# Kernel tuning notes

Measured on AMD Instinct MI355X. Metric: run time of the kernel, lower is better.

## Reference

```python
import jax, jax.numpy as jnp
import numpy as np

DIM = 1024
HEADS = 16
HEAD_DIM = DIM // HEADS
HIDDEN = int(DIM * 4.0)
EPS = 1e-5


def layernorm(x, w, b):
    m = jnp.mean(x, axis=-1, keepdims=True)
    v = jnp.var(x, axis=-1, keepdims=True)
    return (x - m) * jax.lax.rsqrt(v + EPS) * w + b


def apply_rope(t, pos):
    # t: [B, H, S, D], pos: [B, S] int
    half = t.shape[-1] // 2
    inv_freq = 1.0 / (10000.0 ** (jnp.arange(half, dtype=jnp.float32) / half))
    ang = pos.astype(jnp.float32)[:, None, :, None] * inv_freq  # [B,1,S,half]
    cos = jnp.cos(ang)
    sin = jnp.sin(ang)
    t1, t2 = t[..., :half], t[..., half:]
    return jnp.concatenate([t1 * cos - t2 * sin, t2 * cos + t1 * sin], axis=-1)


def setup_inputs() -> dict:
    key = jax.random.key(0)
    ks = jax.random.split(key, 10)
    B, S = 2, 2048
    x = jax.random.normal(ks[0], (B, S, DIM), dtype=jnp.float32)
    pos = jnp.sort(jax.random.randint(ks[1], (B, S), 0, 2048), axis=-1).astype(jnp.int32)
    def lin(k, fi, fo):
        return jax.random.normal(k, (fi, fo), dtype=jnp.float32) / np.sqrt(fi)
    return {
        "x": x,
        "pos": pos,
        "ln1_w": jnp.ones((DIM,), jnp.float32),
        "ln1_b": jnp.zeros((DIM,), jnp.float32),
        "qkv_w": lin(ks[2], DIM, 3 * DIM),
        "qkv_b": jnp.zeros((3 * DIM,), jnp.float32),
        "o_w": lin(ks[3], DIM, DIM),
        "o_b": jnp.zeros((DIM,), jnp.float32),
        "ln2_w": jnp.ones((DIM,), jnp.float32),
        "ln2_b": jnp.zeros((DIM,), jnp.float32),
        "mlp_w1": lin(ks[4], DIM, HIDDEN),
        "mlp_b1": jnp.zeros((HIDDEN,), jnp.float32),
        "mlp_w2": lin(ks[5], HIDDEN, DIM),
        "mlp_b2": jnp.zeros((DIM,), jnp.float32),
    }


def reference(x, pos, ln1_w, ln1_b, qkv_w, qkv_b, o_w, o_b, ln2_w, ln2_b, mlp_w1, mlp_b1, mlp_w2, mlp_b2):
    B, S, C = x.shape
    scale = HEAD_DIM ** -0.5
    xn = layernorm(x, ln1_w, ln1_b)
    qkv = (xn @ qkv_w + qkv_b).reshape(B, S, 3, HEADS, HEAD_DIM)
    qkv = jnp.transpose(qkv, (2, 0, 3, 1, 4))  # [3,B,H,S,D]
    q, k, v = qkv[0], qkv[1], qkv[2]
    q = apply_rope(q, pos)
    k = apply_rope(k, pos)
    scores = jnp.einsum("bhsd,bhtd->bhst", q, k) * scale
    probs = jax.nn.softmax(scores, axis=-1)
    attn = jnp.einsum("bhst,bhtd->bhsd", probs, v)
    attn = jnp.transpose(attn, (0, 2, 1, 3)).reshape(B, S, C)
    x = x + attn @ o_w + o_b
    xn2 = layernorm(x, ln2_w, ln2_b)
    h = jax.nn.gelu(xn2 @ mlp_w1 + mlp_b1, approximate=False)
    x = x + h @ mlp_w2 + mlp_b2
    return x
```

## Files before the change

### kernel.cpp

```cpp
#include <hip/hip_runtime.h>
#include <hip/hip_bf16.h>
#include <math.h>

#define DIMC 1024
#define HEADS 16
#define HD 64
#define HIDDEN 4096
#define BATCH 2
#define SEQ 2048
#define TOK (BATCH*SEQ)

typedef unsigned short u16;
typedef __attribute__((ext_vector_type(8))) short short8;
typedef __attribute__((ext_vector_type(4))) float f32x4;

__device__ __forceinline__ u16 f2bf(float f) {
  unsigned u = __float_as_uint(f);
  u += 0x7fff + ((u >> 16) & 1);
  return (u16)(u >> 16);
}
__device__ __forceinline__ float bf2f(u16 h) {
  return __uint_as_float(((unsigned)h) << 16);
}

__device__ __forceinline__ void gl_lds16(const void* g, void* l) {
  __builtin_amdgcn_global_load_lds(
      (__attribute__((address_space(1))) void*)g,
      (__attribute__((address_space(3))) void*)l, 16, 0, 0);
}

__device__ __forceinline__ const short8* lds_row128(const u16* base, int row, int chunk) {
  return (const short8*)((const char*)base + row * 128 + (((chunk) ^ (row & 7)) << 4));
}

__global__ __launch_bounds__(256) void ln_kernel(
    const float* __restrict__ x, const float* __restrict__ w,
    const float* __restrict__ b, u16* __restrict__ out)
{
  int row = blockIdx.x, tid = threadIdx.x;
  const float4* xr = (const float4*)(x + (size_t)row * DIMC);
  float4 v = xr[tid];
  float s = v.x + v.y + v.z + v.w;
  float s2 = v.x*v.x + v.y*v.y + v.z*v.z + v.w*v.w;
  for (int off = 32; off > 0; off >>= 1) {
    s  += __shfl_down(s, off);
    s2 += __shfl_down(s2, off);
  }
  __shared__ float red[8];
  int lane = tid & 63, wv = tid >> 6;
  if (lane == 0) { red[wv] = s; red[4 + wv] = s2; }
  __syncthreads();
  float S  = red[0] + red[1] + red[2] + red[3];
  float S2 = red[4] + red[5] + red[6] + red[7];
  float mean = S * (1.f / DIMC);
  float var  = S2 * (1.f / DIMC) - mean * mean;
  float inv  = rsqrtf(var + 1e-5f);
  int base = tid * 4;
  float vv[4] = {v.x, v.y, v.z, v.w};
#pragma unroll
  for (int j = 0; j < 4; ++j)
    out[(size_t)row * DIMC + base + j] = f2bf((vv[j] - mean) * inv * w[base + j] + b[base + j]);
}

__global__ __launch_bounds__(256) void transpose_cast(
    const float* __restrict__ W, u16* __restrict__ Wt, int K, int N)
{
  __shared__ float t[32][33];
  int n0 = blockIdx.x * 32, k0 = blockIdx.y * 32;
  for (int r = threadIdx.y; r < 32; r += 8)
    t[r][threadIdx.x] = W[(size_t)(k0 + r) * N + n0 + threadIdx.x];
  __syncthreads();
  for (int r = threadIdx.y; r < 32; r += 8)
    Wt[(size_t)(n0 + r) * K + k0 + threadIdx.x] = f2bf(t[threadIdx.x][r]);
}

template<int EPI, int BM>
__global__ __launch_bounds__(256) void gemm_bt(
    const u16* __restrict__ A, const u16* __restrict__ Bt,
    const float* __restrict__ bias, const float* __restrict__ res,
    u16* __restrict__ outb, float* __restrict__ outf,
    int M, int N, int K)
{
  constexpr int AMM  = BM / 32;
  constexpr int HALF = BM / 2;
  constexpr int AJ   = BM / 32;
  constexpr int ASZ  = BM * 64;
  constexpr int BSZ  = 128 * 64;
  __shared__ u16 shm[(BM + 128) * 64 * 2];
  int tid = threadIdx.x;
  int lane = tid & 63, w = tid >> 6;
  int wr = w >> 1, wc = w & 1;

  int nwg = gridDim.x * gridDim.y;
  int orig = blockIdx.y * gridDim.x + blockIdx.x;
  int wg = (orig & 7) * (nwg >> 3) + (orig >> 3);
  int gi = wg >> 4, wi = wg & 15;
  int gx4 = gridDim.x >> 2;
  int bx = (gi % gx4) * 4 + (wi & 3);
  int by = (gi / gx4) * 4 + (wi >> 2);
  int m0 = by * BM, n0 = bx * 128;

  f32x4 acc[AMM][4] = {};

  int offA[AJ], offB[4];
#pragma unroll
  for (int j = 0; j < AJ; ++j) {
    int p = tid + j * 256, row = p >> 3, cl = (p & 7) ^ (row & 7);
    offA[j] = (m0 + row) * K + cl * 8;
  }
#pragma unroll
  for (int j = 0; j < 4; ++j) {
    int p = tid + j * 256, row = p >> 3, cl = (p & 7) ^ (row & 7);
    offB[j] = (n0 + row) * K + cl * 8;
  }
  int rofs = lane & 15, q4 = lane >> 4;
  int NT = K >> 6;

  auto stage = [&](int buf, int t) {
    u16* Ab = shm + buf * ASZ;
    u16* Bb = shm + 2 * ASZ + buf * BSZ;
#pragma unroll
    for (int j = 0; j < AJ; ++j)
      gl_lds16(A + offA[j] + t * 64, Ab + (tid + j * 256) * 8);
#pragma unroll
    for (int j = 0; j < 4; ++j)
      gl_lds16(Bt + offB[j] + t * 64, Bb + (tid + j * 256) * 8);
  };
  auto compute = [&](int buf) {
    const char* Ab = (const char*)(shm + buf * ASZ);
    const char* Bb = (const char*)(shm + 2 * ASZ + buf * BSZ);
    short8 af[AMM][2], bfr[4][2];
#pragma unroll
    for (int mm = 0; mm < AMM; ++mm)
#pragma unroll
      for (int kk = 0; kk < 2; ++kk) {
        int row = wr * HALF + mm * 16 + rofs;
        af[mm][kk] = *(const short8*)(Ab + row * 128 +
                                      ((((kk << 2) | q4) ^ (row & 7)) << 4));
      }
#pragma unroll
    for (int nn = 0; nn < 4; ++nn)
#pragma unroll
      for (int kk = 0; kk < 2; ++kk) {
        int row = wc * 64 + nn * 16 + rofs;
        bfr[nn][kk] = *(const short8*)(Bb + row * 128 +
                                       ((((kk << 2) | q4) ^ (row & 7)) << 4));
      }
#pragma unroll
    for (int kk = 0; kk < 2; ++kk)
#pragma unroll
      for (int mm = 0; mm < AMM; ++mm)
#pragma unroll
        for (int nn = 0; nn < 4; ++nn)
          acc[mm][nn] = __builtin_amdgcn_mfma_f32_16x16x32_bf16(
              af[mm][kk], bfr[nn][kk], acc[mm][nn], 0, 0, 0);
  };

  stage(0, 0);
  __syncthreads();
  int cur = 0;
  for (int t = 0; t < NT; ++t) {
    if (t + 1 < NT) stage(cur ^ 1, t + 1);
    compute(cur);
    __syncthreads();
    cur ^= 1;
  }

  if (EPI == 0 || EPI == 1) {
    u16* C = shm;
#pragma unroll
    for (int nn = 0; nn < 4; ++nn) {
      int ccol = wc * 64 + nn * 16 + rofs;
      float bv = bias[n0 + ccol];
#pragma unroll
      for (int mm = 0; mm < AMM; ++mm)
#pragma unroll
        for (int r = 0; r < 4; ++r) {
          int crow = wr * HALF + mm * 16 + q4 * 4 + r;
          float v = acc[mm][nn][r] + bv;
          if (EPI == 1) v = 0.5f * v * (1.f + erff(v * 0.70710678118f));
          C[crow * 128 + ccol] = f2bf(v);
        }
    }
    __syncthreads();
    for (int c = tid; c < BM * 16; c += 256) {
      int row = c >> 4, off = (c & 15) * 8;
      *(short8*)(outb + (size_t)(m0 + row) * N + n0 + off) = *(const short8*)&C[row * 128 + off];
    }
  } else {
    float* Cf = (float*)shm;
#pragma unroll
    for (int p = 0; p < 2; ++p) {
      if (wr == p) {
#pragma unroll
        for (int nn = 0; nn < 4; ++nn) {
          int ccol = wc * 64 + nn * 16 + rofs;
          float bv = bias[n0 + ccol];
#pragma unroll
          for (int mm = 0; mm < AMM; ++mm)
#pragma unroll
            for (int r = 0; r < 4; ++r)
              Cf[(mm * 16 + q4 * 4 + r) * 128 + ccol] = acc[mm][nn][r] + bv;
        }
      }
      __syncthreads();
      for (int c = tid; c < HALF * 32; c += 256) {
        int row = c >> 5, off = (c & 31) * 4;
        size_t idx = (size_t)(m0 + p * HALF + row) * N + n0 + off;
        float4 rv = *(const float4*)(res + idx);
        float4 cv = *(const float4*)&Cf[row * 128 + off];
        cv.x += rv.x; cv.y += rv.y; cv.z += rv.z; cv.w += rv.w;
        *(float4*)(outf + idx) = cv;
      }
      __syncthreads();
    }
  }
}

__global__ __launch_bounds__(256) void rope_split(
    const u16* __restrict__ qkv, const int* __restrict__ pos,
    u16* __restrict__ Q, u16* __restrict__ Kk, u16* __restrict__ Vt)
{
  int st = blockIdx.x, bh = blockIdx.y;
  int b = bh >> 4, hh = bh & 15;
  int s0 = st * 64;
  int tid = threadIdx.x;
  __shared__ u16 vtile[64][72];

  for (int i = tid; i < 64 * 32; i += 256) {
    int sl = i >> 5, dp = i & 31;
    int s = s0 + sl;
    float p = (float)pos[b * SEQ + s];
    float freq = exp2f((float)dp * -0.4152410118609203f);
    float ang = p * freq;
    float sn, c;
    __sincosf(ang, &sn, &c);
    const u16* qr = qkv + (size_t)(b * SEQ + s) * 3072 + hh * 64;
    float q1 = bf2f(qr[dp]),        q2 = bf2f(qr[dp + 32]);
    float k1 = bf2f(qr[1024 + dp]), k2 = bf2f(qr[1024 + dp + 32]);
    size_t ob = ((size_t)bh * SEQ + s) * HD;
    const float QS = 0.18033688011112042f;
    Q[ob + dp]       = f2bf((q1 * c - q2 * sn) * QS);
    Q[ob + dp + 32]  = f2bf((q2 * c + q1 * sn) * QS);
    Kk[ob + dp]      = f2bf(k1 * c - k2 * sn);
    Kk[ob + dp + 32] = f2bf(k2 * c + k1 * sn);
  }
  for (int i = tid; i < 64 * 64; i += 256) {
    int sl = i >> 6, d = i & 63;
    vtile[d][sl] = qkv[(size_t)(b * SEQ + s0 + sl) * 3072 + 2048 + hh * 64 + d];
  }
  __syncthreads();
  for (int i = tid; i < 64 * 64; i += 256) {
    int d = i >> 6, sl = i & 63;
    Vt[((size_t)bh * HD + d) * SEQ + s0 + sl] = vtile[d][sl];
  }
}

__global__ __launch_bounds__(256) void attn_kernel(
    const u16* __restrict__ Q, const u16* __restrict__ K,
    const u16* __restrict__ Vt, u16* __restrict__ O)
{
  __shared__ u16 Ks[2][64 * 64];
  __shared__ u16 Vs[2][64 * 64];
  __shared__ u16 Ps[4 * 16 * 64];
  int qt = blockIdx.x, bh = blockIdx.y;
  int b = bh >> 4, hh = bh & 15;
  const u16* Qp = Q + ((size_t)bh * SEQ + qt * 64) * HD;
  const u16* Kp = K + (size_t)bh * SEQ * HD;
  const u16* Vp = Vt + (size_t)bh * HD * SEQ;
  int tid = threadIdx.x, lane = tid & 63, w = tid >> 6;
  int rofs = lane & 15, q4 = lane >> 4;
  int kofs = q4 * 8;

  short8 aq0 = *(const short8*)&Qp[(w * 16 + rofs) * HD + kofs];
  short8 aq1 = *(const short8*)&Qp[(w * 16 + rofs) * HD + 32 + kofs];

  short8 ones;
#pragma unroll
  for (int j = 0; j < 8; ++j) ones[j] = (short)0x3F80;

  f32x4 o[4] = {};
  f32x4 lsum = {};

  int srow = tid >> 3;
  int sg0 = ((tid & 7) ^ (srow & 7)) * 8;
  u16* pw = &Ps[w * 16 * 64];

#define A_STAGE(BUF, T0) do { \
    gl_lds16(Kp + (size_t)((T0) + srow) * HD + sg0, &Ks[BUF][tid * 8]); \
    gl_lds16(Kp + (size_t)((T0) + 32 + srow) * HD + sg0, &Ks[BUF][tid * 8 + 2048]); \
    gl_lds16(Vp + (size_t)srow * SEQ + (T0) + sg0, &Vs[BUF][tid * 8]); \
    gl_lds16(Vp + (size_t)(32 + srow) * SEQ + (T0) + sg0, &Vs[BUF][tid * 8 + 2048]); \
  } while (0)

  auto tile = [&](const u16* KsB, const u16* VsB) {
    f32x4 s[4] = {};
#pragma unroll
    for (int n = 0; n < 4; ++n) {
      int krow = n * 16 + rofs;
      short8 bk0 = *lds_row128(KsB, krow, q4);
      short8 bk1 = *lds_row128(KsB, krow, 4 + q4);
      s[n] = __builtin_amdgcn_mfma_f32_16x16x32_bf16(aq0, bk0, s[n], 0, 0, 0);
      s[n] = __builtin_amdgcn_mfma_f32_16x16x32_bf16(aq1, bk1, s[n], 0, 0, 0);
    }
#pragma unroll
    for (int n = 0; n < 4; ++n)
#pragma unroll
      for (int r = 0; r < 4; ++r) {
        int prow = q4 * 4 + r;
        int pbyte = (n * 16 + rofs) * 2;
        float p = __builtin_amdgcn_exp2f(s[n][r]);
        *(u16*)((char*)pw + prow * 128 + (pbyte ^ ((prow & 7) << 4))) = f2bf(p);
      }
    short8 pa0 = *lds_row128(pw, rofs, q4);
    short8 pa1 = *lds_row128(pw, rofs, 4 + q4);
    lsum = __builtin_amdgcn_mfma_f32_16x16x32_bf16(pa0, ones, lsum, 0, 0, 0);
    lsum = __builtin_amdgcn_mfma_f32_16x16x32_bf16(pa1, ones, lsum, 0, 0, 0);
#pragma unroll
    for (int n = 0; n < 4; ++n) {
      int vrow = n * 16 + rofs;
      short8 bv0 = *lds_row128(VsB, vrow, q4);
      short8 bv1 = *lds_row128(VsB, vrow, 4 + q4);
      o[n] = __builtin_amdgcn_mfma_f32_16x16x32_bf16(pa0, bv0, o[n], 0, 0, 0);
      o[n] = __builtin_amdgcn_mfma_f32_16x16x32_bf16(pa1, bv1, o[n], 0, 0, 0);
    }
  };

  A_STAGE(0, 0);
  __syncthreads();
  for (int t0 = 0; t0 < SEQ; t0 += 128) {
    if (t0 + 64 < SEQ) A_STAGE(1, t0 + 64);
    tile(Ks[0], Vs[0]);
    __syncthreads();
    if (t0 + 128 < SEQ) A_STAGE(0, t0 + 128);
    tile(Ks[1], Vs[1]);
    __syncthreads();
  }
#undef A_STAGE

#pragma unroll
  for (int r = 0; r < 4; ++r) {
    float inv = 1.f / lsum[r];
    int lrow = w * 16 + q4 * 4 + r;
#pragma unroll
    for (int n = 0; n < 4; ++n)
      Ps[lrow * 64 + n * 16 + rofs] = f2bf(o[n][r] * inv);
  }
  __syncthreads();
  for (int c = tid; c < 512; c += 256) {
    int row = c >> 3, off = (c & 7) * 8;
    int sq = qt * 64 + row;
    *(short8*)(O + ((size_t)b * SEQ + sq) * DIMC + hh * 64 + off) = *(const short8*)&Ps[row * 64 + off];
  }
}

extern "C" void kernel_launch(void* const* d_in, const int* in_sizes, int n_in,
                              void* d_out, int out_size, void* d_ws, size_t ws_size,
                              hipStream_t stream) {
  const float* x     = (const float*)d_in[0];
  const int*   pos   = (const int*)  d_in[1];
  const float* ln1_w = (const float*)d_in[2];
  const float* ln1_b = (const float*)d_in[3];
  const float* qkv_w = (const float*)d_in[4];
  const float* qkv_b = (const float*)d_in[5];
  const float* o_w   = (const float*)d_in[6];
  const float* o_b   = (const float*)d_in[7];
  const float* ln2_w = (const float*)d_in[8];
  const float* ln2_b = (const float*)d_in[9];
  const float* w1    = (const float*)d_in[10];
  const float* b1    = (const float*)d_in[11];
  const float* w2    = (const float*)d_in[12];
  const float* b2    = (const float*)d_in[13];
  float* out = (float*)d_out;

  char* ws = (char*)d_ws;
  u16* WqkvT = (u16*)(ws + 0);
  u16* WoT   = (u16*)(ws + 6291456);
  u16* W1T   = (u16*)(ws + 8388608);
  u16* W2T   = (u16*)(ws + 16777216);
  u16* xn    = (u16*)(ws + 25165824);
  u16* qkvbf = (u16*)(ws + 33554432);
  u16* Qb    = (u16*)(ws + 58720256);
  u16* Kb    = (u16*)(ws + 67108864);
  u16* Vtb   = (u16*)(ws + 75497472);
  u16* attnb = (u16*)(ws + 83886080);
  u16* hbuf  = (u16*)(ws + 25165824);
  float* x2  = (float*)(ws + 58720256);
  u16* xn2   = (u16*)(ws + 75497472);

  transpose_cast<<<dim3(3072/32, 1024/32), dim3(32, 8), 0, stream>>>(qkv_w, WqkvT, 1024, 3072);
  transpose_cast<<<dim3(1024/32, 1024/32), dim3(32, 8), 0, stream>>>(o_w,  WoT,  1024, 1024);
  transpose_cast<<<dim3(4096/32, 1024/32), dim3(32, 8), 0, stream>>>(w1,   W1T,  1024, 4096);
  transpose_cast<<<dim3(1024/32, 4096/32), dim3(32, 8), 0, stream>>>(w2,   W2T,  4096, 1024);

  ln_kernel<<<TOK, 256, 0, stream>>>(x, ln1_w, ln1_b, xn);
  gemm_bt<0,128><<<dim3(24, 32), 256, 0, stream>>>(xn, WqkvT, qkv_b, nullptr, qkvbf, nullptr, 4096, 3072, 1024);
  rope_split<<<dim3(32, 32), 256, 0, stream>>>(qkvbf, pos, Qb, Kb, Vtb);
  attn_kernel<<<dim3(32, 32), 256, 0, stream>>>(Qb, Kb, Vtb, attnb);
  gemm_bt<2,64><<<dim3(8, 64), 256, 0, stream>>>(attnb, WoT, o_b, x, nullptr, x2, 4096, 1024, 1024);
  ln_kernel<<<TOK, 256, 0, stream>>>(x2, ln2_w, ln2_b, xn2);
  gemm_bt<1,128><<<dim3(32, 32), 256, 0, stream>>>(xn2, W1T, b1, nullptr, hbuf, nullptr, 4096, 4096, 1024);
  gemm_bt<2,64><<<dim3(8, 64), 256, 0, stream>>>(hbuf, W2T, b2, x2, nullptr, out, 4096, 1024, 4096);
}
```

Measured before the change: 256.6 us.

## Add 256x256-tile 8-wave GEMM with XCD-aware remap for QKV and MLP-up

Adds a new gemm8p kernel using 512 threads, 256x256 output tiles, XOR-swizzled LDS filled by direct global-to-LDS loads, and a phased pipeline that interleaves half-K staging with MFMA compute under explicit waitcnt and barrier control. Workgroup IDs are remapped across the 8 XCDs and grouped into 4x4 supertiles to improve L2 reuse. The QKV and first MLP GEMMs now use it, and the old gemm_bt keeps only the residual epilogue. The larger tile raises arithmetic intensity, but with one block per CU the grids of 192 and 256 blocks may fill the machine unevenly, and the hand-tuned waitcnt counts are fragile.

```diff
diff --git a/kernel.cpp b/kernel.cpp
--- a/kernel.cpp
+++ b/kernel.cpp
@@ -72,6 +72,118 @@
   __syncthreads();
   for (int r = threadIdx.y; r < 32; r += 8)
     Wt[(size_t)(n0 + r) * K + k0 + threadIdx.x] = f2bf(t[threadIdx.x][r]);
+}
+
+template<int EPI>
+__global__ __launch_bounds__(512, 1) void gemm8p(
+    const u16* __restrict__ A, const u16* __restrict__ Bt,
+    const float* __restrict__ bias, u16* __restrict__ outb,
+    int M, int N, int K)
+{
+  __shared__ u16 lds[2][2][2][256 * 32];
+  int tid = threadIdx.x;
+  int lane = tid & 63, wid = tid >> 6;
+  int wr = wid >> 2, wn = wid & 3;
+  int rofs = lane & 15, q4 = lane >> 4;
+
+  int nwg = gridDim.x * gridDim.y;
+  int orig = blockIdx.y * gridDim.x + blockIdx.x;
+  int wg = (orig & 7) * (nwg >> 3) + (orig >> 3);
+  int gi = wg >> 4, wi = wg & 15;
+  int gx4 = gridDim.x >> 2;
+  int bx = (gi % gx4) * 4 + (wi & 3);
+  int by = (gi / gx4) * 4 + (wi >> 2);
+  int m0 = by * 256, n0 = bx * 256;
+  int mb = wr * 128, nb = wn * 64;
+
+  f32x4 acc[8][4] = {};
+
+  int p0 = tid, p1 = tid + 512;
+  int r0 = p0 >> 2, c0 = ((p0 & 3) ^ (r0 & 3)) * 8;
+  int r1 = p1 >> 2, c1 = ((p1 & 3) ^ (r1 & 3)) * 8;
+  size_t aoff0 = (size_t)(m0 + r0) * K + c0, aoff1 = (size_t)(m0 + r1) * K + c1;
+  size_t boff0 = (size_t)(n0 + r0) * K + c0, boff1 = (size_t)(n0 + r1) * K + c1;
+
+#define STAGE_A(D_, H_, KC_) do { \
+    gl_lds16(A + aoff0 + (KC_), &lds[D_][0][H_][tid * 8]); \
+    gl_lds16(A + aoff1 + (KC_), &lds[D_][0][H_][(tid + 512) * 8]); } while (0)
+#define STAGE_B(D_, H_, KC_) do { \
+    gl_lds16(Bt + boff0 + (KC_), &lds[D_][1][H_][tid * 8]); \
+    gl_lds16(Bt + boff1 + (KC_), &lds[D_][1][H_][(tid + 512) * 8]); } while (0)
+
+#define PH_COMP(D_, H_, MG_) do { \
+    const char* Ab = (const char*)&lds[D_][0][H_][0]; \
+    const char* Bb = (const char*)&lds[D_][1][H_][0]; \
+    short8 a_[4], b_[4]; \
+    _Pragma("unroll") for (int mm = 0; mm < 4; ++mm) { \
+      int row = mb + ((MG_) * 4 + mm) * 16 + rofs; \
+      a_[mm] = *(const short8*)(Ab + row * 64 + ((q4 ^ (row & 3)) << 4)); \
+    } \
+    _Pragma("unroll") for (int nn = 0; nn < 4; ++nn) { \
+      int row = nb + nn * 16 + rofs; \
+      b_[nn] = *(const short8*)(Bb + row * 64 + ((q4 ^ (row & 3)) << 4)); \
+    } \
+    __builtin_amdgcn_s_setprio(1); \
+    _Pragma("unroll") for (int mm = 0; mm < 4; ++mm) \
+      _Pragma("unroll") for (int nn = 0; nn < 4; ++nn) \
+        acc[(MG_) * 4 + mm][nn] = __builtin_amdgcn_mfma_f32_16x16x32_bf16( \
+            a_[mm], b_[nn], acc[(MG_) * 4 + mm][nn], 0, 0, 0); \
+    __builtin_amdgcn_s_setprio(0); } while (0)
+
+#define VMW(N_) asm volatile("s_waitcnt vmcnt(" #N_ ")" ::: "memory")
+#define SBAR()  do { __builtin_amdgcn_s_barrier(); asm volatile("" ::: "memory"); } while (0)
+
+  int NT = K >> 6;
+  STAGE_A(0, 0, 0); STAGE_B(0, 0, 0); STAGE_A(0, 1, 32); STAGE_B(0, 1, 32);
+
+  for (int t = 0; t < NT; ++t) {
+    int d = t & 1, nx = d ^ 1;
+    int kc = (t + 1) * 64;
+    bool st = (t + 1 < NT);
+    if (st) { STAGE_A(nx, 0, kc); VMW(6); } else { VMW(4); }
+    SBAR();
+    PH_COMP(d, 0, 0);
+    SBAR();
+    if (st) STAGE_B(nx, 0, kc);
+    SBAR();
+    PH_COMP(d, 0, 1);
+    SBAR();
+    if (st) { STAGE_A(nx, 1, kc + 32); VMW(6); } else { VMW(0); }
+    SBAR();
+    PH_COMP(d, 1, 0);
+    SBAR();
+    if (st) STAGE_B(nx, 1, kc + 32);
+    SBAR();
+    PH_COMP(d, 1, 1);
+    SBAR();
+  }
+#undef STAGE_A
+#undef STAGE_B
+#undef PH_COMP
+#undef VMW
+#undef SBAR
+
+  __syncthreads();
+  u16* Ct = &lds[0][0][0][0];
+#pragma unroll
+  for (int nn = 0; nn < 4; ++nn) {
+    int ccol = nb + nn * 16 + rofs;
+    float bv = bias[n0 + ccol];
+#pragma unroll
+    for (int m = 0; m < 8; ++m)
+#pragma unroll
+      for (int r = 0; r < 4; ++r) {
+        int row = mb + m * 16 + q4 * 4 + r;
+        float v = acc[m][nn][r] + bv;
+        if (EPI == 1) v = 0.5f * v * (1.f + erff(v * 0.70710678118f));
+        Ct[row * 256 + ccol] = f2bf(v);
+      }
+  }
+  __syncthreads();
+  for (int c = tid; c < 256 * 32; c += 512) {
+    int row = c >> 5, offb = (c & 31) * 8;
+    *(short8*)(outb + (size_t)(m0 + row) * N + n0 + offb) = *(const short8*)&Ct[row * 256 + offb];
+  }
 }
 
 template<int EPI, int BM>
@@ -166,54 +278,31 @@
     cur ^= 1;
   }
 
-  if (EPI == 0 || EPI == 1) {
-    u16* C = shm;
-#pragma unroll
-    for (int nn = 0; nn < 4; ++nn) {
-      int ccol = wc * 64 + nn * 16 + rofs;
-      float bv = bias[n0 + ccol];
-#pragma unroll
-      for (int mm = 0; mm < AMM; ++mm)
-#pragma unroll
-        for (int r = 0; r < 4; ++r) {
-          int crow = wr * HALF + mm * 16 + q4 * 4 + r;
-          float v = acc[mm][nn][r] + bv;
-          if (EPI == 1) v = 0.5f * v * (1.f + erff(v * 0.70710678118f));
-          C[crow * 128 + ccol] = f2bf(v);
-        }
+  float* Cf = (float*)shm;
+#pragma unroll
+  for (int p = 0; p < 2; ++p) {
+    if (wr == p) {
+#pragma unroll
+      for (int nn = 0; nn < 4; ++nn) {
+        int ccol = wc * 64 + nn * 16 + rofs;
+        float bv = bias[n0 + ccol];
+#pragma unroll
+        for (int mm = 0; mm < AMM; ++mm)
+#pragma unroll
+          for (int r = 0; r < 4; ++r)
+            Cf[(mm * 16 + q4 * 4 + r) * 128 + ccol] = acc[mm][nn][r] + bv;
+      }
     }
     __syncthreads();
-    for (int c = tid; c < BM * 16; c += 256) {
-      int row = c >> 4, off = (c & 15) * 8;
-      *(short8*)(outb + (size_t)(m0 + row) * N + n0 + off) = *(const short8*)&C[row * 128 + off];
+    for (int c = tid; c < HALF * 32; c += 256) {
+      int row = c >> 5, off = (c & 31) * 4;
+      size_t idx = (size_t)(m0 + p * HALF + row) * N + n0 + off;
+      float4 rv = *(const float4*)(res + idx);
+      float4 cv = *(const float4*)&Cf[row * 128 + off];
+      cv.x += rv.x; cv.y += rv.y; cv.z += rv.z; cv.w += rv.w;
+      *(float4*)(outf + idx) = cv;
     }
-  } else {
-    float* Cf = (float*)shm;
-#pragma unroll
-    for (int p = 0; p < 2; ++p) {
-      if (wr == p) {
-#pragma unroll
-        for (int nn = 0; nn < 4; ++nn) {
-          int ccol = wc * 64 + nn * 16 + rofs;
-          float bv = bias[n0 + ccol];
-#pragma unroll
-          for (int mm = 0; mm < AMM; ++mm)
-#pragma unroll
-            for (int r = 0; r < 4; ++r)
-              Cf[(mm * 16 + q4 * 4 + r) * 128 + ccol] = acc[mm][nn][r] + bv;
-        }
-      }
-      __syncthreads();
-      for (int c = tid; c < HALF * 32; c += 256) {
-        int row = c >> 5, off = (c & 31) * 4;
-        size_t idx = (size_t)(m0 + p * HALF + row) * N + n0 + off;
-        float4 rv = *(const float4*)(res + idx);
-        float4 cv = *(const float4*)&Cf[row * 128 + off];
-        cv.x += rv.x; cv.y += rv.y; cv.z += rv.z; cv.w += rv.w;
-        *(float4*)(outf + idx) = cv;
-      }
-      __syncthreads();
-    }
+    __syncthreads();
   }
 }
 
@@ -394,11 +483,11 @@
   transpose_cast<<<dim3(1024/32, 4096/32), dim3(32, 8), 0, stream>>>(w2,   W2T,  4096, 1024);
 
   ln_kernel<<<TOK, 256, 0, stream>>>(x, ln1_w, ln1_b, xn);
-  gemm_bt<0,128><<<dim3(24, 32), 256, 0, stream>>>(xn, WqkvT, qkv_b, nullptr, qkvbf, nullptr, 4096, 3072, 1024);
+  gemm8p<0><<<dim3(12, 16), 512, 0, stream>>>(xn, WqkvT, qkv_b, qkvbf, 4096, 3072, 1024);
   rope_split<<<dim3(32, 32), 256, 0, stream>>>(qkvbf, pos, Qb, Kb, Vtb);
   attn_kernel<<<dim3(32, 32), 256, 0, stream>>>(Qb, Kb, Vtb, attnb);
   gemm_bt<2,64><<<dim3(8, 64), 256, 0, stream>>>(attnb, WoT, o_b, x, nullptr, x2, 4096, 1024, 1024);
   ln_kernel<<<TOK, 256, 0, stream>>>(x2, ln2_w, ln2_b, xn2);
-  gemm_bt<1,128><<<dim3(32, 32), 256, 0, stream>>>(xn2, W1T, b1, nullptr, hbuf, nullptr, 4096, 4096, 1024);
+  gemm8p<1><<<dim3(16, 16), 512, 0, stream>>>(xn2, W1T, b1, hbuf, 4096, 4096, 1024);
   gemm_bt<2,64><<<dim3(8, 64), 256, 0, stream>>>(hbuf, W2T, b2, x2, nullptr, out, 4096, 1024, 4096);
 }
```

Result: slower. 279.1 us (+8.8%).

## Double query tile per attention block and split GEMMs into specialized kernels

Applied to the files above, without the earlier changes.

The attention kernel now handles 128 query rows per block instead of 64, so each K/V tile loaded into LDS is reused by twice as many query rows, and it halves the grid. The 128-row GEMMs (QKV, MLP1) are rewritten as a single-buffered loop with one LDS buffer, in place of the double-buffered stage/compute pipeline. The residual GEMMs are moved into separately named kernels. In exchange, attention carries more accumulator registers per wave and fewer blocks, and the QKV/MLP1 GEMMs lose their overlap of global loads with compute but use less LDS, which may allow higher occupancy.

```diff
diff --git a/kernel.cpp b/kernel.cpp
--- a/kernel.cpp
+++ b/kernel.cpp
@@ -74,19 +74,118 @@
     Wt[(size_t)(n0 + r) * K + k0 + threadIdx.x] = f2bf(t[threadIdx.x][r]);
 }
 
-template<int EPI, int BM>
-__global__ __launch_bounds__(256) void gemm_bt(
+template<int GELU>
+__device__ __forceinline__ void gemm_lin_body(
+    u16* shm, const u16* __restrict__ A, const u16* __restrict__ Bt,
+    const float* __restrict__ bias, u16* __restrict__ outb, int M, int N, int K)
+{
+  int tid = threadIdx.x;
+  int lane = tid & 63, w = tid >> 6;
+  int wr = w >> 1, wc = w & 1;
+
+  int nwg = gridDim.x * gridDim.y;
+  int orig = blockIdx.y * gridDim.x + blockIdx.x;
+  int wg = (orig & 7) * (nwg >> 3) + (orig >> 3);
+  int gi = wg >> 4, wi = wg & 15;
+  int gx4 = gridDim.x >> 2;
+  int bx = (gi % gx4) * 4 + (wi & 3);
+  int by = (gi / gx4) * 4 + (wi >> 2);
+  int m0 = by * 128, n0 = bx * 128;
+
+  f32x4 acc[4][4] = {};
+
+  int offA[4], offB[4];
+#pragma unroll
+  for (int j = 0; j < 4; ++j) {
+    int p = tid + j * 256, row = p >> 3, cl = (p & 7) ^ (row & 7);
+    offA[j] = (m0 + row) * K + cl * 8;
+    offB[j] = (n0 + row) * K + cl * 8;
+  }
+  int rofs = lane & 15, q4 = lane >> 4;
+  int NT = K >> 6;
+  u16* Bs = shm + 128 * 64;
+
+  for (int t = 0; t < NT; ++t) {
+#pragma unroll
+    for (int j = 0; j < 4; ++j) {
+      gl_lds16(A + offA[j] + t * 64, shm + (tid + j * 256) * 8);
+      gl_lds16(Bt + offB[j] + t * 64, Bs + (tid + j * 256) * 8);
+    }
+    __syncthreads();
+    {
+      short8 af[4][2], bfr[4][2];
+#pragma unroll
+      for (int mm = 0; mm < 4; ++mm)
+#pragma unroll
+        for (int kk = 0; kk < 2; ++kk) {
+          int row = wr * 64 + mm * 16 + rofs;
+          af[mm][kk] = *(const short8*)((const char*)shm + row * 128 +
+                                        ((((kk << 2) | q4) ^ (row & 7)) << 4));
+        }
+#pragma unroll
+      for (int nn = 0; nn < 4; ++nn)
+#pragma unroll
+        for (int kk = 0; kk < 2; ++kk) {
+          int row = wc * 64 + nn * 16 + rofs;
+          bfr[nn][kk] = *(const short8*)((const char*)Bs + row * 128 +
+                                         ((((kk << 2) | q4) ^ (row & 7)) << 4));
+        }
+#pragma unroll
+      for (int kk = 0; kk < 2; ++kk)
+#pragma unroll
+        for (int mm = 0; mm < 4; ++mm)
+#pragma unroll
+          for (int nn = 0; nn < 4; ++nn)
+            acc[mm][nn] = __builtin_amdgcn_mfma_f32_16x16x32_bf16(
+                af[mm][kk], bfr[nn][kk], acc[mm][nn], 0, 0, 0);
+    }
+    __syncthreads();
+  }
+
+  u16* C = shm;
+#pragma unroll
+  for (int nn = 0; nn < 4; ++nn) {
+    int ccol = wc * 64 + nn * 16 + rofs;
+    float bv = bias[n0 + ccol];
+#pragma unroll
+    for (int mm = 0; mm < 4; ++mm)
+#pragma unroll
+      for (int r = 0; r < 4; ++r) {
+        int crow = wr * 64 + mm * 16 + q4 * 4 + r;
+        float v = acc[mm][nn][r] + bv;
+        if (GELU) v = 0.5f * v * (1.f + erff(v * 0.70710678118f));
+        C[crow * 128 + ccol] = f2bf(v);
+      }
+  }
+  __syncthreads();
+  for (int c = tid; c < 128 * 16; c += 256) {
+    int row = c >> 4, off = (c & 15) * 8;
+    *(short8*)(outb + (size_t)(m0 + row) * N + n0 + off) = *(const short8*)&C[row * 128 + off];
+  }
+}
+
+__global__ __launch_bounds__(256) void gemm_qkv(
     const u16* __restrict__ A, const u16* __restrict__ Bt,
+    const float* __restrict__ bias, u16* __restrict__ outb, int M, int N, int K)
+{
+  __shared__ u16 shm[128 * 64 * 2];
+  gemm_lin_body<0>(shm, A, Bt, bias, outb, M, N, K);
+}
+__global__ __launch_bounds__(256) void gemm_mlp1(
+    const u16* __restrict__ A, const u16* __restrict__ Bt,
+    const float* __restrict__ bias, u16* __restrict__ outb, int M, int N, int K)
+{
+  __shared__ u16 shm[128 * 64 * 2];
+  gemm_lin_body<1>(shm, A, Bt, bias, outb, M, N, K);
+}
+
+__device__ __forceinline__ void gemm_res_body(
+    u16* shm, const u16* __restrict__ A, const u16* __restrict__ Bt,
     const float* __restrict__ bias, const float* __restrict__ res,
-    u16* __restrict__ outb, float* __restrict__ outf,
-    int M, int N, int K)
-{
-  constexpr int AMM  = BM / 32;
-  constexpr int HALF = BM / 2;
-  constexpr int AJ   = BM / 32;
-  constexpr int ASZ  = BM * 64;
-  constexpr int BSZ  = 128 * 64;
-  __shared__ u16 shm[(BM + 128) * 64 * 2];
+    float* __restrict__ outf, int M, int N, int K)
+{
+  constexpr int BM = 64, AMM = 2, HALF = 32, AJ = 2;
+  constexpr int ASZ = BM * 64, BSZ = 128 * 64;
   int tid = threadIdx.x;
   int lane = tid & 63, w = tid >> 6;
   int wr = w >> 1, wc = w & 1;
@@ -166,55 +265,49 @@
     cur ^= 1;
   }
 
-  if (EPI == 0 || EPI == 1) {
-    u16* C = shm;
-#pragma unroll
-    for (int nn = 0; nn < 4; ++nn) {
-      int ccol = wc * 64 + nn * 16 + rofs;
-      float bv = bias[n0 + ccol];
-#pragma unroll
-      for (int mm = 0; mm < AMM; ++mm)
-#pragma unroll
-        for (int r = 0; r < 4; ++r) {
-          int crow = wr * HALF + mm * 16 + q4 * 4 + r;
-          float v = acc[mm][nn][r] + bv;
-          if (EPI == 1) v = 0.5f * v * (1.f + erff(v * 0.70710678118f));
-          C[crow * 128 + ccol] = f2bf(v);
-        }
-    }
-    __syncthreads();
-    for (int c = tid; c < BM * 16; c += 256) {
-      int row = c >> 4, off = (c & 15) * 8;
-      *(short8*)(outb + (size_t)(m0 + row) * N + n0 + off) = *(const short8*)&C[row * 128 + off];
-    }
-  } else {
-    float* Cf = (float*)shm;
-#pragma unroll
-    for (int p = 0; p < 2; ++p) {
-      if (wr == p) {
-#pragma unroll
-        for (int nn = 0; nn < 4; ++nn) {
-          int ccol = wc * 64 + nn * 16 + rofs;
-          float bv = bias[n0 + ccol];
-#pragma unroll
-          for (int mm = 0; mm < AMM; ++mm)
-#pragma unroll
-            for (int r = 0; r < 4; ++r)
-              Cf[(mm * 16 + q4 * 4 + r) * 128 + ccol] = acc[mm][nn][r] + bv;
-        }
+  float* Cf = (float*)shm;
+#pragma unroll
+  for (int p = 0; p < 2; ++p) {
+    if (wr == p) {
+#pragma unroll
+      for (int nn = 0; nn < 4; ++nn) {
+        int ccol = wc * 64 + nn * 16 + rofs;
+        float bv = bias[n0 + ccol];
+#pragma unroll
+        for (int mm = 0; mm < AMM; ++mm)
+#pragma unroll
+          for (int r = 0; r < 4; ++r)
+            Cf[(mm * 16 + q4 * 4 + r) * 128 + ccol] = acc[mm][nn][r] + bv;
       }
-      __syncthreads();
-      for (int c = tid; c < HALF * 32; c += 256) {
-        int row = c >> 5, off = (c & 31) * 4;
-        size_t idx = (size_t)(m0 + p * HALF + row) * N + n0 + off;
-        float4 rv = *(const float4*)(res + idx);
-        float4 cv = *(const float4*)&Cf[row * 128 + off];
-        cv.x += rv.x; cv.y += rv.y; cv.z += rv.z; cv.w += rv.w;
-        *(float4*)(outf + idx) = cv;
-      }
-      __syncthreads();
-    }
-  }
+    }
+    __syncthreads();
+    for (int c = tid; c < HALF * 32; c += 256) {
+      int row = c >> 5, off = (c & 31) * 4;
+      size_t idx = (size_t)(m0 + p * HALF + row) * N + n0 + off;
+      float4 rv = *(const float4*)(res + idx);
+      float4 cv = *(const float4*)&Cf[row * 128 + off];
+      cv.x += rv.x; cv.y += rv.y; cv.z += rv.z; cv.w += rv.w;
+      *(float4*)(outf + idx) = cv;
+    }
+    __syncthreads();
+  }
+}
+
+__global__ __launch_bounds__(256) void gemm_oproj(
+    const u16* __restrict__ A, const u16* __restrict__ Bt,
+    const float* __restrict__ bias, const float* __restrict__ res,
+    float* __restrict__ outf, int M, int N, int K)
+{
+  __shared__ u16 shm[(64 + 128) * 64 * 2];
+  gemm_res_body(shm, A, Bt, bias, res, outf, M, N, K);
+}
+__global__ __launch_bounds__(256) void gemm_mlp2(
+    const u16* __restrict__ A, const u16* __restrict__ Bt,
+    const float* __restrict__ bias, const float* __restrict__ res,
+    float* __restrict__ outf, int M, int N, int K)
+{
+  __shared__ u16 shm[(64 + 128) * 64 * 2];
+  gemm_res_body(shm, A, Bt, bias, res, outf, M, N, K);
 }
 
 __global__ __launch_bounds__(256) void rope_split(
@@ -256,35 +349,39 @@
   }
 }
 
-__global__ __launch_bounds__(256) void attn_kernel(
+__global__ __launch_bounds__(256) void attn128(
     const u16* __restrict__ Q, const u16* __restrict__ K,
     const u16* __restrict__ Vt, u16* __restrict__ O)
 {
   __shared__ u16 Ks[2][64 * 64];
   __shared__ u16 Vs[2][64 * 64];
-  __shared__ u16 Ps[4 * 16 * 64];
+  __shared__ u16 Ps[4 * 32 * 64];
   int qt = blockIdx.x, bh = blockIdx.y;
   int b = bh >> 4, hh = bh & 15;
-  const u16* Qp = Q + ((size_t)bh * SEQ + qt * 64) * HD;
+  const u16* Qp = Q + ((size_t)bh * SEQ + qt * 128) * HD;
   const u16* Kp = K + (size_t)bh * SEQ * HD;
   const u16* Vp = Vt + (size_t)bh * HD * SEQ;
   int tid = threadIdx.x, lane = tid & 63, w = tid >> 6;
   int rofs = lane & 15, q4 = lane >> 4;
   int kofs = q4 * 8;
 
-  short8 aq0 = *(const short8*)&Qp[(w * 16 + rofs) * HD + kofs];
-  short8 aq1 = *(const short8*)&Qp[(w * 16 + rofs) * HD + 32 + kofs];
+  short8 aq[2][2];
+#pragma unroll
+  for (int m = 0; m < 2; ++m)
+#pragma unroll
+    for (int h = 0; h < 2; ++h)
+      aq[m][h] = *(const short8*)&Qp[(m * 64 + w * 16 + rofs) * HD + h * 32 + kofs];
 
   short8 ones;
 #pragma unroll
   for (int j = 0; j < 8; ++j) ones[j] = (short)0x3F80;
 
-  f32x4 o[4] = {};
-  f32x4 lsum = {};
+  f32x4 o[2][4] = {};
+  f32x4 lsum[2] = {};
 
   int srow = tid >> 3;
   int sg0 = ((tid & 7) ^ (srow & 7)) * 8;
-  u16* pw = &Ps[w * 16 * 64];
+  u16* pw = &Ps[w * 32 * 64];
 
 #define A_STAGE(BUF, T0) do { \
     gl_lds16(Kp + (size_t)((T0) + srow) * HD + sg0, &Ks[BUF][tid * 8]); \
@@ -294,35 +391,54 @@
   } while (0)
 
   auto tile = [&](const u16* KsB, const u16* VsB) {
-    f32x4 s[4] = {};
+    f32x4 s[2][4] = {};
+    short8 bk0[4], bk1[4];
 #pragma unroll
     for (int n = 0; n < 4; ++n) {
       int krow = n * 16 + rofs;
-      short8 bk0 = *lds_row128(KsB, krow, q4);
-      short8 bk1 = *lds_row128(KsB, krow, 4 + q4);
-      s[n] = __builtin_amdgcn_mfma_f32_16x16x32_bf16(aq0, bk0, s[n], 0, 0, 0);
-      s[n] = __builtin_amdgcn_mfma_f32_16x16x32_bf16(aq1, bk1, s[n], 0, 0, 0);
-    }
-#pragma unroll
-    for (int n = 0; n < 4; ++n)
-#pragma unroll
-      for (int r = 0; r < 4; ++r) {
-        int prow = q4 * 4 + r;
-        int pbyte = (n * 16 + rofs) * 2;
-        float p = __builtin_amdgcn_exp2f(s[n][r]);
-        *(u16*)((char*)pw + prow * 128 + (pbyte ^ ((prow & 7) << 4))) = f2bf(p);
+      bk0[n] = *lds_row128(KsB, krow, q4);
+      bk1[n] = *lds_row128(KsB, krow, 4 + q4);
+    }
+#pragma unroll
+    for (int m = 0; m < 2; ++m)
+#pragma unroll
+      for (int n = 0; n < 4; ++n) {
+        s[m][n] = __builtin_amdgcn_mfma_f32_16x16x32_bf16(aq[m][0], bk0[n], s[m][n], 0, 0, 0);
+        s[m][n] = __builtin_amdgcn_mfma_f32_16x16x32_bf16(aq[m][1], bk1[n], s[m][n], 0, 0, 0);
       }
-    short8 pa0 = *lds_row128(pw, rofs, q4);
-    short8 pa1 = *lds_row128(pw, rofs, 4 + q4);
-    lsum = __builtin_amdgcn_mfma_f32_16x16x32_bf16(pa0, ones, lsum, 0, 0, 0);
-    lsum = __builtin_amdgcn_mfma_f32_16x16x32_bf16(pa1, ones, lsum, 0, 0, 0);
+#pragma unroll
+    for (int m = 0; m < 2; ++m)
+#pragma unroll
+      for (int n = 0; n < 4; ++n)
+#pragma unroll
+        for (int r = 0; r < 4; ++r) {
+          int prow = m * 16 + q4 * 4 + r;
+          int pbyte = (n * 16 + rofs) * 2;
+          float p = __builtin_amdgcn_exp2f(s[m][n][r]);
+          *(u16*)((char*)pw + prow * 128 + (pbyte ^ ((prow & 7) << 4))) = f2bf(p);
+        }
+    short8 pa[2][2];
+#pragma unroll
+    for (int m = 0; m < 2; ++m) {
+      pa[m][0] = *lds_row128(pw, m * 16 + rofs, q4);
+      pa[m][1] = *lds_row128(pw, m * 16 + rofs, 4 + q4);
+    }
+    short8 bv0[4], bv1[4];
 #pragma unroll
     for (int n = 0; n < 4; ++n) {
       int vrow = n * 16 + rofs;
-      short8 bv0 = *lds_row128(VsB, vrow, q4);
-      short8 bv1 = *lds_row128(VsB, vrow, 4 + q4);
-      o[n] = __builtin_amdgcn_mfma_f32_16x16x32_bf16(pa0, bv0, o[n], 0, 0, 0);
-      o[n] = __builtin_amdgcn_mfma_f32_16x16x32_bf16(pa1, bv1, o[n], 0, 0, 0);
+      bv0[n] = *lds_row128(VsB, vrow, q4);
+      bv1[n] = *lds_row128(VsB, vrow, 4 + q4);
+    }
+#pragma unroll
+    for (int m = 0; m < 2; ++m) {
+      lsum[m] = __builtin_amdgcn_mfma_f32_16x16x32_bf16(pa[m][0], ones, lsum[m], 0, 0, 0);
+      lsum[m] = __builtin_amdgcn_mfma_f32_16x16x32_bf16(pa[m][1], ones, lsum[m], 0, 0, 0);
+#pragma unroll
+      for (int n = 0; n < 4; ++n) {
+        o[m][n] = __builtin_amdgcn_mfma_f32_16x16x32_bf16(pa[m][0], bv0[n], o[m][n], 0, 0, 0);
+        o[m][n] = __builtin_amdgcn_mfma_f32_16x16x32_bf16(pa[m][1], bv1[n], o[m][n], 0, 0, 0);
+      }
     }
   };
 
@@ -339,17 +455,19 @@
 #undef A_STAGE
 
 #pragma unroll
-  for (int r = 0; r < 4; ++r) {
-    float inv = 1.f / lsum[r];
-    int lrow = w * 16 + q4 * 4 + r;
-#pragma unroll
-    for (int n = 0; n < 4; ++n)
-      Ps[lrow * 64 + n * 16 + rofs] = f2bf(o[n][r] * inv);
-  }
-  __syncthreads();
-  for (int c = tid; c < 512; c += 256) {
+  for (int m = 0; m < 2; ++m)
+#pragma unroll
+    for (int r = 0; r < 4; ++r) {
+      float inv = 1.f / lsum[m][r];
+      int rr = m * 64 + w * 16 + q4 * 4 + r;
+#pragma unroll
+      for (int n = 0; n < 4; ++n)
+        Ps[rr * 64 + n * 16 + rofs] = f2bf(o[m][n][r] * inv);
+    }
+  __syncthreads();
+  for (int c = tid; c < 128 * 8; c += 256) {
     int row = c >> 3, off = (c & 7) * 8;
-    int sq = qt * 64 + row;
+    int sq = qt * 128 + row;
     *(short8*)(O + ((size_t)b * SEQ + sq) * DIMC + hh * 64 + off) = *(const short8*)&Ps[row * 64 + off];
   }
 }
@@ -394,11 +512,11 @@
   transpose_cast<<<dim3(1024/32, 4096/32), dim3(32, 8), 0, stream>>>(w2,   W2T,  4096, 1024);
 
   ln_kernel<<<TOK, 256, 0, stream>>>(x, ln1_w, ln1_b, xn);
-  gemm_bt<0,128><<<dim3(24, 32), 256, 0, stream>>>(xn, WqkvT, qkv_b, nullptr, qkvbf, nullptr, 4096, 3072, 1024);
+  gemm_qkv<<<dim3(24, 32), 256, 0, stream>>>(xn, WqkvT, qkv_b, qkvbf, 4096, 3072, 1024);
   rope_split<<<dim3(32, 32), 256, 0, stream>>>(qkvbf, pos, Qb, Kb, Vtb);
-  attn_kernel<<<dim3(32, 32), 256, 0, stream>>>(Qb, Kb, Vtb, attnb);
-  gemm_bt<2,64><<<dim3(8, 64), 256, 0, stream>>>(attnb, WoT, o_b, x, nullptr, x2, 4096, 1024, 1024);
+  attn128<<<dim3(16, 32), 256, 0, stream>>>(Qb, Kb, Vtb, attnb);
+  gemm_oproj<<<dim3(8, 64), 256, 0, stream>>>(attnb, WoT, o_b, x, x2, 4096, 1024, 1024);
   ln_kernel<<<TOK, 256, 0, stream>>>(x2, ln2_w, ln2_b, xn2);
-  gemm_bt<1,128><<<dim3(32, 32), 256, 0, stream>>>(xn2, W1T, b1, nullptr, hbuf, nullptr, 4096, 4096, 1024);
-  gemm_bt<2,64><<<dim3(8, 64), 256, 0, stream>>>(hbuf, W2T, b2, x2, nullptr, out, 4096, 1024, 4096);
-}
+  gemm_mlp1<<<dim3(32, 32), 256, 0, stream>>>(xn2, W1T, b1, hbuf, 4096, 4096, 1024);
+  gemm_mlp2<<<dim3(8, 64), 256, 0, stream>>>(hbuf, W2T, b2, x2, out, 4096, 1024, 4096);
+}
```

Result: no change. 257.2 us (+0.2%).
